# Kernel tuning notes

Measured on AMD Instinct MI355X. Metric: run time of the kernel, lower is better.

The kernel has to match this reference:

```python
import jax, jax.numpy as jnp
import numpy as np

D, M, N = 1024, 16, 16384
H = D // M  # head dim = 64
C = 10.0    # tanh logit clipping


def setup_inputs() -> dict:
    key = jax.random.key(0)
    kb, kq, km, k1, k2, k3, k4 = jax.random.split(key, 7)
    def xavier(k, shape):
        # torch xavier_uniform: fan_in = prod(shape[1:]), fan_out = shape[0]*prod(shape[2:])
        fan_in = int(np.prod(shape[1:]))
        fan_out = shape[0] * int(np.prod(shape[2:]))
        bound = float(np.sqrt(6.0 / (fan_in + fan_out)))
        return jax.random.uniform(k, shape, jnp.float32, -bound, bound)
    return {
        "b": jax.random.normal(kb, (N, D), jnp.float32),
        "q_s_bar": jax.random.normal(kq, (D,), jnp.float32),
        "mask": jax.random.randint(km, (N,), 0, 2).astype(bool),
        "W_k_bar": xavier(k1, (M, H, D)),
        "W_v_bar": xavier(k2, (M, H, D)),
        "W_k": xavier(k3, (D, D)),
        "W_q": xavier(k4, (D, D)),
    }


def reference(b, q_s_bar, mask, W_k_bar, W_v_bar, W_k, W_q):
    # k_bar, v_bar: (N, M, H)  == matmul(W, b.t()).permute(2,0,1)
    k_bar = jnp.einsum('mhd,nd->nmh', W_k_bar, b)
    v_bar = jnp.einsum('mhd,nd->nmh', W_v_bar, b)
    k = b @ W_k.T                      # (N, D) == matmul(W_k, b.t()).t()
    q = q_s_bar.reshape(M, H)          # (M, H)
    # c_bar: (N, M, M) == matmul(k_bar, q.T) / sqrt(h)
    c_bar = jnp.einsum('nmh,gh->nmg', k_bar, q) / np.float32(np.sqrt(H))
    scores = jnp.where(mask[:, None, None], c_bar, -jnp.inf)
    attn = jax.nn.softmax(scores, axis=0)          # softmax over N
    # (N,M,M) @ (N,M,H) batched -> (N,M,H); view(N,-1).sum(0) -> (D,)
    q_s = jnp.einsum('nmg,ngh->nmh', attn, v_bar).reshape(N, D).sum(0)
    c = (k @ (W_q @ q_s)) / np.float32(np.sqrt(D))  # (N,)
    c = C * jnp.tanh(c)
    return jnp.where(mask, c, -jnp.inf)
```

## Files before the change

kernel.cpp:

```cpp
#include <hip/hip_runtime.h>
#include <math.h>
#include <float.h>

#define NN 16384
#define DD 1024
#define MM 16
#define HH 64
#define MG 256

typedef __attribute__((ext_vector_type(8))) short bh8;
typedef __attribute__((ext_vector_type(4))) float f32x4;

__device__ inline float bf2f(unsigned short u) {
    union { unsigned int i; float f; } v;
    v.i = ((unsigned int)u) << 16;
    return v.f;
}

__device__ inline unsigned short f2bf(float f) {
    union { float f; unsigned int i; } v;
    v.f = f;
    unsigned int r = v.i + 0x7FFFu + ((v.i >> 16) & 1u);
    return (unsigned short)(r >> 16);
}

__device__ inline float ld1(const void* p, long i, int isf) {
    return isf ? ((const float*)p)[i] : bf2f(((const unsigned short*)p)[i]);
}

__device__ inline float4 ld4(const void* p, long i, int isf) {
    if (isf) return *(const float4*)((const float*)p + i);
    ushort4 u = *(const ushort4*)((const unsigned short*)p + i);
    return make_float4(bf2f(u.x), bf2f(u.y), bf2f(u.z), bf2f(u.w));
}

__device__ inline bool get_mask(const unsigned char* mp, int n, int flag) {
    return flag ? (mp[n] != 0) : (mp[4 * n] != 0);
}

__device__ inline void gl_lds16(const void* g, void* l) {
    __builtin_amdgcn_global_load_lds(
        (const __attribute__((address_space(1))) unsigned int*)g,
        (__attribute__((address_space(3))) unsigned int*)l, 16, 0, 0);
}

__global__ void detect(const unsigned char* __restrict__ mp,
                       const unsigned char* __restrict__ bb, int* flags,
                       float* __restrict__ u) {
    int i = blockIdx.x * 256 + threadIdx.x;
    if (i < DD) u[i] = 0.f;
    int v1 = ((i & 3) != 0 && mp[i] != 0) ? 1 : 0;
    unsigned char c = bb[4 * i + 1];
    bool expish = (c == 0x00) || (c == 0x80) || (c >= 0x30 && c <= 0x47) ||
                  (c >= 0xB0 && c <= 0xC7);
    int v2 = expish ? 0 : 1;
    unsigned long long b1 = __ballot(v1);
    unsigned long long b2 = __ballot(v2);
    if ((threadIdx.x & 63) == 0) {
        if (b1) atomicOr(&flags[0], 1);
        if (b2) atomicOr(&flags[1], 1);
    }
}

__global__ void fold_k(const void* __restrict__ Wkb, const void* __restrict__ qsb,
                       unsigned short* __restrict__ Abf, const int* __restrict__ flags) {
    __shared__ float q[DD];
    int isf = flags[1];
    int m = blockIdx.x;
    int d = blockIdx.y * 128 + threadIdx.x;
    for (int i = threadIdx.x; i < DD; i += 128) q[i] = ld1(qsb, i, isf);
    __syncthreads();
    float acc[MM];
#pragma unroll
    for (int g = 0; g < MM; g++) acc[g] = 0.f;
    for (int h = 0; h < HH; h++) {
        float w = ld1(Wkb, (long)(m * HH + h) * DD + d, isf);
#pragma unroll
        for (int g = 0; g < MM; g++) acc[g] += w * q[g * HH + h];
    }
#pragma unroll
    for (int g = 0; g < MM; g++)
        Abf[(long)(m * MM + g) * DD + d] = f2bf(acc[g] * 0.125f);
}

__global__ void cvt_b(const void* __restrict__ bB, unsigned short* __restrict__ bbf,
                      unsigned short* __restrict__ bT, const int* __restrict__ flags) {
    __shared__ unsigned short tl[64 * 72];
    int isf = flags[1];
    int bn = blockIdx.x, bd = blockIdx.y;
    int t = threadIdx.x;
    int i0 = t >> 4, jg = t & 15;
#pragma unroll
    for (int it = 0; it < 4; ++it) {
        int i = i0 + it * 16;
        long gidx = (long)(bn * 64 + i) * DD + bd * 64 + jg * 4;
        ushort4 o;
        if (isf) {
            float4 v = *(const float4*)((const float*)bB + gidx);
            o.x = f2bf(v.x); o.y = f2bf(v.y); o.z = f2bf(v.z); o.w = f2bf(v.w);
        } else {
            o = *(const ushort4*)((const unsigned short*)bB + gidx);
        }
        *(ushort4*)&bbf[gidx] = o;
        *(ushort4*)&tl[i * 72 + jg * 4] = o;
    }
    __syncthreads();
    int p = t >> 2, g = t & 3;
#pragma unroll
    for (int k = 0; k < 4; ++k) {
        int nl = g * 4 + k * 16;
        ushort4 o;
        o.x = tl[(nl + 0) * 72 + p];
        o.y = tl[(nl + 1) * 72 + p];
        o.z = tl[(nl + 2) * 72 + p];
        o.w = tl[(nl + 3) * 72 + p];
        *(ushort4*)&bT[(long)(bd * 64 + p) * NN + bn * 64 + nl] = o;
    }
}

__global__ __launch_bounds__(256) void gemm_b_mfma(
    const unsigned short* __restrict__ Abf, const unsigned short* __restrict__ bbf,
    const unsigned char* __restrict__ mp, const int* __restrict__ flags,
    unsigned short* __restrict__ Cb) {
    __shared__ __align__(16) unsigned short As[128 * 64];
    __shared__ __align__(16) unsigned short Bs[64 * 64];
    int m0 = blockIdx.x * 128, n0 = blockIdx.y * 64;
    int t = threadIdx.x;
    int lane = t & 63, w = t >> 6;
    int wm = w >> 1, wn = w & 1;
    int r = lane & 15, q = lane >> 4;
    f32x4 acc[4][2] = {};
    for (int k0 = 0; k0 < DD; k0 += 64) {
#pragma unroll
        for (int i = 0; i < 4; i++) {
            int L = (i * 4 + w) * 64 + lane;
            int row = L >> 3, c = (L & 7) ^ (row & 7);
            gl_lds16(&Abf[(long)(m0 + row) * DD + k0 + c * 8], &As[(i * 4 + w) * 512]);
        }
#pragma unroll
        for (int i = 0; i < 2; i++) {
            int L = (i * 4 + w) * 64 + lane;
            int row = L >> 3, c = (L & 7) ^ (row & 7);
            gl_lds16(&bbf[(long)(n0 + row) * DD + k0 + c * 8], &Bs[(i * 4 + w) * 512]);
        }
        __syncthreads();
#pragma unroll
        for (int h = 0; h < 2; h++) {
            bh8 af[4], bfr[2];
#pragma unroll
            for (int fi = 0; fi < 4; fi++) {
                int row = wm * 64 + fi * 16 + r;
                int ck = (h * 4 + q) ^ (row & 7);
                af[fi] = *(const bh8*)&As[row * 64 + ck * 8];
            }
#pragma unroll
            for (int fj = 0; fj < 2; fj++) {
                int row = wn * 32 + fj * 16 + r;
                int ck = (h * 4 + q) ^ (row & 7);
                bfr[fj] = *(const bh8*)&Bs[row * 64 + ck * 8];
            }
#pragma unroll
            for (int fi = 0; fi < 4; fi++)
#pragma unroll
                for (int fj = 0; fj < 2; fj++)
                    acc[fi][fj] = __builtin_amdgcn_mfma_f32_16x16x32_bf16(
                        af[fi], bfr[fj], acc[fi][fj], 0, 0, 0);
        }
        __syncthreads();
    }
    int mflag = flags[0];
#pragma unroll
    for (int fj = 0; fj < 2; fj++) {
        int gn = n0 + wn * 32 + fj * 16 + r;
        float nb = get_mask(mp, gn, mflag) ? 0.f : -INFINITY;
#pragma unroll
        for (int fi = 0; fi < 4; fi++)
#pragma unroll
            for (int reg = 0; reg < 4; reg++) {
                int gm = m0 + wm * 64 + fi * 16 + q * 4 + reg;
                Cb[(long)gm * NN + gn] = f2bf(acc[fi][fj][reg] + nb);
            }
    }
}

__global__ void softmax_part(const unsigned short* __restrict__ Cb,
                             float* __restrict__ sws) {
    __shared__ float red[256];
    int mg = blockIdx.x, z = blockIdx.y, t = threadIdx.x;
    bh8 v8 = *(const bh8*)&Cb[(long)mg * NN + z * 2048 + t * 8];
    float x[8];
#pragma unroll
    for (int j = 0; j < 8; j++) x[j] = bf2f((unsigned short)v8[j]);
    float mx = x[0];
#pragma unroll
    for (int j = 1; j < 8; j++) mx = fmaxf(mx, x[j]);
    red[t] = mx;
    __syncthreads();
    for (int s = 128; s; s >>= 1) {
        if (t < s) red[t] = fmaxf(red[t], red[t + s]);
        __syncthreads();
    }
    mx = red[0];
    __syncthreads();
    float sm = 0.f;
#pragma unroll
    for (int j = 0; j < 8; j++) sm += expf(x[j] - mx);
    red[t] = sm;
    __syncthreads();
    for (int s = 128; s; s >>= 1) {
        if (t < s) red[t] += red[t + s];
        __syncthreads();
    }
    if (t == 0) {
        sws[(mg * 8 + z) * 2] = mx;
        sws[(mg * 8 + z) * 2 + 1] = red[0];
    }
}

__global__ void softmax_norm(const unsigned short* __restrict__ Cb,
                             const float* __restrict__ sws,
                             unsigned short* __restrict__ P) {
    int mg = blockIdx.x, z = blockIdx.y, t = threadIdx.x;
    float mx = -INFINITY;
#pragma unroll
    for (int z2 = 0; z2 < 8; z2++) mx = fmaxf(mx, sws[(mg * 8 + z2) * 2]);
    float S = 0.f;
#pragma unroll
    for (int z2 = 0; z2 < 8; z2++) {
        float pm = sws[(mg * 8 + z2) * 2], ps = sws[(mg * 8 + z2) * 2 + 1];
        if (pm > -INFINITY) S += ps * expf(pm - mx);
    }
    float inv = 1.0f / S;
    long i = (long)mg * NN + z * 2048 + t * 8;
    bh8 v8 = *(const bh8*)&Cb[i];
    bh8 o;
#pragma unroll
    for (int j = 0; j < 8; j++)
        o[j] = (short)f2bf(expf(bf2f((unsigned short)v8[j]) - mx) * inv);
    *(bh8*)&P[i] = o;
}

__global__ __launch_bounds__(256) void gemm_d_mfma(
    const unsigned short* __restrict__ P, const unsigned short* __restrict__ bT,
    unsigned short* __restrict__ Tpart) {
    __shared__ __align__(16) unsigned short As[128 * 64];
    __shared__ __align__(16) unsigned short Bs[64 * 64];
    int m0 = blockIdx.x * 128, d0 = blockIdx.y * 64;
    long kbase = (long)blockIdx.z * 1024;
    unsigned short* Cg = Tpart + (long)blockIdx.z * (MG * DD);
    int t = threadIdx.x;
    int lane = t & 63, w = t >> 6;
    int wm = w >> 1, wn = w & 1;
    int r = lane & 15, q = lane >> 4;
    f32x4 acc[4][2] = {};
    for (int k0 = 0; k0 < 1024; k0 += 64) {
#pragma unroll
        for (int i = 0; i < 4; i++) {
            int L = (i * 4 + w) * 64 + lane;
            int row = L >> 3, c = (L & 7) ^ (row & 7);
            gl_lds16(&P[(long)(m0 + row) * NN + kbase + k0 + c * 8], &As[(i * 4 + w) * 512]);
        }
#pragma unroll
        for (int i = 0; i < 2; i++) {
            int L = (i * 4 + w) * 64 + lane;
            int row = L >> 3, c = (L & 7) ^ (row & 7);
            gl_lds16(&bT[(long)(d0 + row) * NN + kbase + k0 + c * 8], &Bs[(i * 4 + w) * 512]);
        }
        __syncthreads();
#pragma unroll
        for (int h = 0; h < 2; h++) {
            bh8 af[4], bfr[2];
#pragma unroll
            for (int fi = 0; fi < 4; fi++) {
                int row = wm * 64 + fi * 16 + r;
                int ck = (h * 4 + q) ^ (row & 7);
                af[fi] = *(const bh8*)&As[row * 64 + ck * 8];
            }
#pragma unroll
            for (int fj = 0; fj < 2; fj++) {
                int row = wn * 32 + fj * 16 + r;
                int ck = (h * 4 + q) ^ (row & 7);
                bfr[fj] = *(const bh8*)&Bs[row * 64 + ck * 8];
            }
#pragma unroll
            for (int fi = 0; fi < 4; fi++)
#pragma unroll
                for (int fj = 0; fj < 2; fj++)
                    acc[fi][fj] = __builtin_amdgcn_mfma_f32_16x16x32_bf16(
                        af[fi], bfr[fj], acc[fi][fj], 0, 0, 0);
        }
        __syncthreads();
    }
#pragma unroll
    for (int fi = 0; fi < 4; fi++)
#pragma unroll
        for (int fj = 0; fj < 2; fj++)
#pragma unroll
            for (int reg = 0; reg < 4; reg++) {
                int gm = m0 + wm * 64 + fi * 16 + q * 4 + reg;
                int gd = d0 + wn * 32 + fj * 16 + r;
                Cg[(long)gm * DD + gd] = f2bf(acc[fi][fj][reg]);
            }
}

__global__ void reduce_T(const unsigned short* __restrict__ Tpart, float* __restrict__ T) {
    long i = (long)(blockIdx.x * 256 + threadIdx.x) * 8;
    float s[8] = {};
#pragma unroll
    for (int c = 0; c < 16; c++) {
        bh8 v = *(const bh8*)&Tpart[(long)c * (MG * DD) + i];
#pragma unroll
        for (int j = 0; j < 8; j++) s[j] += bf2f((unsigned short)v[j]);
    }
    *(float4*)&T[i] = make_float4(s[0], s[1], s[2], s[3]);
    *(float4*)&T[i + 4] = make_float4(s[4], s[5], s[6], s[7]);
}

__global__ void fold_v(const void* __restrict__ Wvb, const float* __restrict__ T,
                       float* __restrict__ qs, const int* __restrict__ flags) {
    int isf = flags[1];
    int w = threadIdx.x >> 6, lane = threadIdx.x & 63;
    int o = blockIdx.x * 4 + w;
    int m = o >> 6, h = o & 63;
    float s = 0.f;
    for (int g = 0; g < MM; g++) {
        const float* Trow = T + (long)(m * MM + g) * DD;
        long wbase = (long)(g * HH + h) * DD;
#pragma unroll
        for (int k = 0; k < 4; k++) {
            int d = lane * 4 + k * 256;
            float4 tv = *(const float4*)&Trow[d];
            float4 wv = ld4(Wvb, wbase + d, isf);
            s += wv.x * tv.x + wv.y * tv.y + wv.z * tv.z + wv.w * tv.w;
        }
    }
    for (int off = 32; off; off >>= 1) s += __shfl_down(s, off, 64);
    if (lane == 0) qs[o] = s;
}

__global__ void matvec_rows(const void* __restrict__ W, const float* __restrict__ x,
                            float* __restrict__ y, const int* __restrict__ flags) {
    int isf = flags[1];
    int lane = threadIdx.x & 63;
    int r = blockIdx.x * 4 + (threadIdx.x >> 6);
    long base = (long)r * DD;
    float s = 0.f;
#pragma unroll
    for (int k = 0; k < 4; k++) {
        int j = lane * 4 + k * 256;
        float4 wv = ld4(W, base + j, isf);
        float4 xv = *(const float4*)&x[j];
        s += wv.x * xv.x + wv.y * xv.y + wv.z * xv.z + wv.w * xv.w;
    }
    for (int off = 32; off; off >>= 1) s += __shfl_down(s, off, 64);
    if (lane == 0) y[r] = s;
}

__global__ void matvec_col(const void* __restrict__ Wk, const float* __restrict__ w1,
                           float* __restrict__ u, const int* __restrict__ flags) {
    __shared__ float xs[16];
    int isf = flags[1];
    int d = blockIdx.x * 256 + threadIdx.x;
    int i0 = blockIdx.y * 16;
    if (threadIdx.x < 16) xs[threadIdx.x] = w1[i0 + threadIdx.x];
    __syncthreads();
    float s = 0.f;
#pragma unroll
    for (int ii = 0; ii < 16; ii++) s += ld1(Wk, (long)(i0 + ii) * DD + d, isf) * xs[ii];
    atomicAdd(&u[d], s);
}

__global__ void final_k(const unsigned short* __restrict__ bbf, const float* __restrict__ u,
                        const unsigned char* __restrict__ mp, const int* __restrict__ flags,
                        void* __restrict__ out) {
    int mflag = flags[0];
    int isf = flags[1];
    int n = blockIdx.x * 4 + (threadIdx.x >> 6);
    int lane = threadIdx.x & 63;
    const unsigned short* row = bbf + (long)n * DD;
    float s = 0.f;
#pragma unroll
    for (int k = 0; k < 4; k++) {
        int j = lane * 4 + k * 256;
        ushort4 v = *(const ushort4*)&row[j];
        float4 uu = *(const float4*)&u[j];
        s += bf2f(v.x) * uu.x + bf2f(v.y) * uu.y + bf2f(v.z) * uu.z + bf2f(v.w) * uu.w;
    }
    for (int off = 32; off; off >>= 1) s += __shfl_down(s, off, 64);
    if (lane == 0) {
        float c = 10.f * tanhf(s * (1.0f / 32.0f));
        bool mk = get_mask(mp, n, mflag);
        if (isf) {
            union { unsigned int i; float f; } vv;
            vv.i = mk ? (((unsigned int)f2bf(c)) << 16) : 0xFF7F0000u;
            ((float*)out)[n] = vv.f;
        } else {
            ((unsigned short*)out)[n] = mk ? f2bf(c) : (unsigned short)0xFF7F;
        }
    }
}

extern "C" void kernel_launch(void* const* d_in, const int* in_sizes, int n_in,
                              void* d_out, int out_size, void* d_ws, size_t ws_size,
                              hipStream_t stream) {
    const void* b = d_in[0];
    const void* qsb = d_in[1];
    const unsigned char* mp = (const unsigned char*)d_in[2];
    const void* Wkb = d_in[3];
    const void* Wvb = d_in[4];
    const void* Wk = d_in[5];
    const void* Wq = d_in[6];

    char* ws = (char*)d_ws;
    unsigned short* bbf = (unsigned short*)(ws);
    unsigned short* bT = (unsigned short*)(ws + (32u << 20));
    unsigned short* Cb = (unsigned short*)(ws + (64u << 20));
    unsigned short* Tpart = (unsigned short*)(ws + (72u << 20));
    unsigned short* P = (unsigned short*)(ws + (80u << 20));
    unsigned short* Abf = (unsigned short*)(ws + (88u << 20));
    float* T = (float*)(ws + (89u << 20));
    float* small = (float*)(ws + (90u << 20));
    float* qs = small;
    float* w1 = qs + 1024;
    float* u = w1 + 1024;
    float* sws = u + 1024;
    int* flags = (int*)(sws + 4096);

    hipMemsetAsync(flags, 0, 2 * sizeof(int), stream);

    detect<<<64, 256, 0, stream>>>(mp, (const unsigned char*)b, flags, u);
    fold_k<<<dim3(16, 8), 128, 0, stream>>>(Wkb, qsb, Abf, flags);
    cvt_b<<<dim3(256, 16), 256, 0, stream>>>(b, bbf, bT, flags);
    gemm_b_mfma<<<dim3(2, 256), 256, 0, stream>>>(Abf, bbf, mp, flags, Cb);
    softmax_part<<<dim3(256, 8), 256, 0, stream>>>(Cb, sws);
    softmax_norm<<<dim3(256, 8), 256, 0, stream>>>(Cb, sws, P);
    gemm_d_mfma<<<dim3(2, 16, 16), 256, 0, stream>>>(P, bT, Tpart);
    reduce_T<<<128, 256, 0, stream>>>(Tpart, T);
    fold_v<<<256, 256, 0, stream>>>(Wvb, T, qs, flags);
    matvec_rows<<<256, 256, 0, stream>>>(Wq, qs, w1, flags);
    matvec_col<<<dim3(4, 64), 256, 0, stream>>>(Wk, w1, u, flags);
    final_k<<<4096, 256, 0, stream>>>(bbf, u, mp, flags, d_out);
}
```

Measured before the change: 228.5 us.

## Fuse softmax partial statistics into score GEMM epilogue and retile transpose kernel

The score GEMM epilogue now computes per-row max and sum-of-exp for each 64-column tile using wave shuffles and shared memory, and writes them to a stats buffer. This removes the softmax_part kernel and its full re-read of the score matrix. softmax_norm reduces the 256 partials per row before normalizing. Separately, cvt_b is retiled to 128 rows per block with wider per-thread loads and stores, which halves the grid. The cost is a heavier GEMM epilogue, with extra exps and a block sync.

```diff
diff --git a/kernel.cpp b/kernel.cpp
--- a/kernel.cpp
+++ b/kernel.cpp
@@ -85,46 +85,56 @@
 
 __global__ void cvt_b(const void* __restrict__ bB, unsigned short* __restrict__ bbf,
                       unsigned short* __restrict__ bT, const int* __restrict__ flags) {
-    __shared__ unsigned short tl[64 * 72];
+    __shared__ unsigned short tl[128 * 68];
     int isf = flags[1];
     int bn = blockIdx.x, bd = blockIdx.y;
     int t = threadIdx.x;
-    int i0 = t >> 4, jg = t & 15;
-#pragma unroll
-    for (int it = 0; it < 4; ++it) {
-        int i = i0 + it * 16;
-        long gidx = (long)(bn * 64 + i) * DD + bd * 64 + jg * 4;
+    int row = t >> 1, half = (t & 1) * 32;
+    long gbase = (long)(bn * 128 + row) * DD + bd * 64 + half;
+    ushort4 ov[8];
+    if (isf) {
+        const float* src = (const float*)bB + gbase;
+        float4 f[8];
+#pragma unroll
+        for (int k = 0; k < 8; k++) f[k] = *(const float4*)(src + k * 4);
+#pragma unroll
+        for (int k = 0; k < 8; k++) {
+            ov[k].x = f2bf(f[k].x); ov[k].y = f2bf(f[k].y);
+            ov[k].z = f2bf(f[k].z); ov[k].w = f2bf(f[k].w);
+        }
+    } else {
+        const unsigned short* src = (const unsigned short*)bB + gbase;
+#pragma unroll
+        for (int k = 0; k < 8; k++) ov[k] = *(const ushort4*)(src + k * 4);
+    }
+#pragma unroll
+    for (int k = 0; k < 8; k++) {
+        *(ushort4*)&bbf[gbase + k * 4] = ov[k];
+        *(ushort4*)&tl[row * 68 + half + k * 4] = ov[k];
+    }
+    __syncthreads();
+    int p = t & 63, nb = (t >> 6) * 32;
+    long obase = (long)(bd * 64 + p) * NN + bn * 128 + nb;
+#pragma unroll
+    for (int k = 0; k < 8; k++) {
+        int n4 = nb + k * 4;
         ushort4 o;
-        if (isf) {
-            float4 v = *(const float4*)((const float*)bB + gidx);
-            o.x = f2bf(v.x); o.y = f2bf(v.y); o.z = f2bf(v.z); o.w = f2bf(v.w);
-        } else {
-            o = *(const ushort4*)((const unsigned short*)bB + gidx);
-        }
-        *(ushort4*)&bbf[gidx] = o;
-        *(ushort4*)&tl[i * 72 + jg * 4] = o;
-    }
-    __syncthreads();
-    int p = t >> 2, g = t & 3;
-#pragma unroll
-    for (int k = 0; k < 4; ++k) {
-        int nl = g * 4 + k * 16;
-        ushort4 o;
-        o.x = tl[(nl + 0) * 72 + p];
-        o.y = tl[(nl + 1) * 72 + p];
-        o.z = tl[(nl + 2) * 72 + p];
-        o.w = tl[(nl + 3) * 72 + p];
-        *(ushort4*)&bT[(long)(bd * 64 + p) * NN + bn * 64 + nl] = o;
+        o.x = tl[(n4 + 0) * 68 + p];
+        o.y = tl[(n4 + 1) * 68 + p];
+        o.z = tl[(n4 + 2) * 68 + p];
+        o.w = tl[(n4 + 3) * 68 + p];
+        *(ushort4*)&bT[obase + k * 4] = o;
     }
 }
 
 __global__ __launch_bounds__(256) void gemm_b_mfma(
     const unsigned short* __restrict__ Abf, const unsigned short* __restrict__ bbf,
     const unsigned char* __restrict__ mp, const int* __restrict__ flags,
-    unsigned short* __restrict__ Cb) {
+    unsigned short* __restrict__ Cb, float2* __restrict__ sws2) {
     __shared__ __align__(16) unsigned short As[128 * 64];
     __shared__ __align__(16) unsigned short Bs[64 * 64];
-    int m0 = blockIdx.x * 128, n0 = blockIdx.y * 64;
+    __shared__ float lstat[2][64][2][2];
+    int mg0 = blockIdx.x * 128, n0 = blockIdx.y * 64;
     int t = threadIdx.x;
     int lane = t & 63, w = t >> 6;
     int wm = w >> 1, wn = w & 1;
@@ -135,7 +145,7 @@
         for (int i = 0; i < 4; i++) {
             int L = (i * 4 + w) * 64 + lane;
             int row = L >> 3, c = (L & 7) ^ (row & 7);
-            gl_lds16(&Abf[(long)(m0 + row) * DD + k0 + c * 8], &As[(i * 4 + w) * 512]);
+            gl_lds16(&Abf[(long)(mg0 + row) * DD + k0 + c * 8], &As[(i * 4 + w) * 512]);
         }
 #pragma unroll
         for (int i = 0; i < 2; i++) {
@@ -169,74 +179,74 @@
         __syncthreads();
     }
     int mflag = flags[0];
+    float nbv[2];
 #pragma unroll
     for (int fj = 0; fj < 2; fj++) {
         int gn = n0 + wn * 32 + fj * 16 + r;
-        float nb = get_mask(mp, gn, mflag) ? 0.f : -INFINITY;
-#pragma unroll
-        for (int fi = 0; fi < 4; fi++)
-#pragma unroll
-            for (int reg = 0; reg < 4; reg++) {
-                int gm = m0 + wm * 64 + fi * 16 + q * 4 + reg;
-                Cb[(long)gm * NN + gn] = f2bf(acc[fi][fj][reg] + nb);
-            }
-    }
-}
-
-__global__ void softmax_part(const unsigned short* __restrict__ Cb,
-                             float* __restrict__ sws) {
+        nbv[fj] = get_mask(mp, gn, mflag) ? 0.f : -INFINITY;
+    }
+#pragma unroll
+    for (int fi = 0; fi < 4; fi++)
+#pragma unroll
+        for (int reg = 0; reg < 4; reg++) {
+            float x0 = acc[fi][0][reg] + nbv[0];
+            float x1 = acc[fi][1][reg] + nbv[1];
+            int gm = mg0 + wm * 64 + fi * 16 + q * 4 + reg;
+            Cb[(long)gm * NN + n0 + wn * 32 + 0 * 16 + r] = f2bf(x0);
+            Cb[(long)gm * NN + n0 + wn * 32 + 1 * 16 + r] = f2bf(x1);
+            float m = fmaxf(x0, x1);
+#pragma unroll
+            for (int d = 1; d <= 8; d <<= 1) m = fmaxf(m, __shfl_xor(m, d, 64));
+            float e = 0.f;
+            if (m > -INFINITY) e = expf(x0 - m) + expf(x1 - m);
+#pragma unroll
+            for (int d = 1; d <= 8; d <<= 1) e += __shfl_xor(e, d, 64);
+            if (r == 0) {
+                int rowl = fi * 16 + q * 4 + reg;
+                lstat[wm][rowl][wn][0] = m;
+                lstat[wm][rowl][wn][1] = e;
+            }
+        }
+    __syncthreads();
+    if (t < 128) {
+        int wmi = t >> 6, rowl = t & 63;
+        float ma = lstat[wmi][rowl][0][0], sa = lstat[wmi][rowl][0][1];
+        float mb = lstat[wmi][rowl][1][0], sb = lstat[wmi][rowl][1][1];
+        float m = fmaxf(ma, mb);
+        float ssum = 0.f;
+        if (ma > -INFINITY) ssum += sa * expf(ma - m);
+        if (mb > -INFINITY) ssum += sb * expf(mb - m);
+        sws2[(long)(mg0 + wmi * 64 + rowl) * 256 + blockIdx.y] = make_float2(m, ssum);
+    }
+}
+
+__global__ void softmax_norm(const unsigned short* __restrict__ Cb,
+                             const float2* __restrict__ sws2,
+                             unsigned short* __restrict__ P) {
     __shared__ float red[256];
     int mg = blockIdx.x, z = blockIdx.y, t = threadIdx.x;
-    bh8 v8 = *(const bh8*)&Cb[(long)mg * NN + z * 2048 + t * 8];
-    float x[8];
-#pragma unroll
-    for (int j = 0; j < 8; j++) x[j] = bf2f((unsigned short)v8[j]);
-    float mx = x[0];
-#pragma unroll
-    for (int j = 1; j < 8; j++) mx = fmaxf(mx, x[j]);
-    red[t] = mx;
+    float2 st = sws2[(long)mg * 256 + t];
+    red[t] = st.x;
     __syncthreads();
     for (int s = 128; s; s >>= 1) {
         if (t < s) red[t] = fmaxf(red[t], red[t + s]);
         __syncthreads();
     }
-    mx = red[0];
-    __syncthreads();
-    float sm = 0.f;
-#pragma unroll
-    for (int j = 0; j < 8; j++) sm += expf(x[j] - mx);
-    red[t] = sm;
+    float M = red[0];
+    __syncthreads();
+    red[t] = (st.x > -INFINITY) ? st.y * expf(st.x - M) : 0.f;
     __syncthreads();
     for (int s = 128; s; s >>= 1) {
         if (t < s) red[t] += red[t + s];
         __syncthreads();
     }
-    if (t == 0) {
-        sws[(mg * 8 + z) * 2] = mx;
-        sws[(mg * 8 + z) * 2 + 1] = red[0];
-    }
-}
-
-__global__ void softmax_norm(const unsigned short* __restrict__ Cb,
-                             const float* __restrict__ sws,
-                             unsigned short* __restrict__ P) {
-    int mg = blockIdx.x, z = blockIdx.y, t = threadIdx.x;
-    float mx = -INFINITY;
-#pragma unroll
-    for (int z2 = 0; z2 < 8; z2++) mx = fmaxf(mx, sws[(mg * 8 + z2) * 2]);
-    float S = 0.f;
-#pragma unroll
-    for (int z2 = 0; z2 < 8; z2++) {
-        float pm = sws[(mg * 8 + z2) * 2], ps = sws[(mg * 8 + z2) * 2 + 1];
-        if (pm > -INFINITY) S += ps * expf(pm - mx);
-    }
-    float inv = 1.0f / S;
+    float inv = 1.0f / red[0];
     long i = (long)mg * NN + z * 2048 + t * 8;
     bh8 v8 = *(const bh8*)&Cb[i];
     bh8 o;
 #pragma unroll
     for (int j = 0; j < 8; j++)
-        o[j] = (short)f2bf(expf(bf2f((unsigned short)v8[j]) - mx) * inv);
+        o[j] = (short)f2bf(expf(bf2f((unsigned short)v8[j]) - M) * inv);
     *(bh8*)&P[i] = o;
 }
 
@@ -423,17 +433,16 @@
     float* qs = small;
     float* w1 = qs + 1024;
     float* u = w1 + 1024;
-    float* sws = u + 1024;
-    int* flags = (int*)(sws + 4096);
+    int* flags = (int*)(u + 1024);
+    float2* sws2 = (float2*)(ws + (91u << 20));
 
     hipMemsetAsync(flags, 0, 2 * sizeof(int), stream);
 
     detect<<<64, 256, 0, stream>>>(mp, (const unsigned char*)b, flags, u);
     fold_k<<<dim3(16, 8), 128, 0, stream>>>(Wkb, qsb, Abf, flags);
-    cvt_b<<<dim3(256, 16), 256, 0, stream>>>(b, bbf, bT, flags);
-    gemm_b_mfma<<<dim3(2, 256), 256, 0, stream>>>(Abf, bbf, mp, flags, Cb);
-    softmax_part<<<dim3(256, 8), 256, 0, stream>>>(Cb, sws);
-    softmax_norm<<<dim3(256, 8), 256, 0, stream>>>(Cb, sws, P);
+    cvt_b<<<dim3(128, 16), 256, 0, stream>>>(b, bbf, bT, flags);
+    gemm_b_mfma<<<dim3(2, 256), 256, 0, stream>>>(Abf, bbf, mp, flags, Cb, sws2);
+    softmax_norm<<<dim3(256, 8), 256, 0, stream>>>(Cb, sws2, P);
     gemm_d_mfma<<<dim3(2, 16, 16), 256, 0, stream>>>(P, bT, Tpart);
     reduce_T<<<128, 256, 0, stream>>>(Tpart, T);
     fold_v<<<256, 256, 0, stream>>>(Wvb, T, qs, flags);
```

After: 237.8 us. 4.1% more time.
